# Kernel optimization log

Hardware: AMD Instinct MI355X
Metric: run time of the kernel (lower is better)

The kernel has to match this reference:

```python
import jax, jax.numpy as jnp
import numpy as np

N = 50000
E = 800000
IN, HID, OUT = 256, 64, 64
H1, H2 = 4, 1
SLOPE = 0.2  # DGL GATConv default negative_slope


def setup_inputs() -> dict:
    key = jax.random.key(0)
    ks = jax.random.split(key, 12)
    inp = {
        "features": jax.random.normal(ks[0], (N, IN), jnp.float32),
        "src": jax.random.randint(ks[1], (E,), 0, N),
        "dst": jax.random.randint(ks[2], (E,), 0, N),
        # layer 1 params (fc has no bias in DGL; separate bias added post-aggregation)
        "W1": jax.random.normal(ks[3], (IN, H1 * HID), jnp.float32) * (1.0 / np.sqrt(IN)),
        "al1": jax.random.normal(ks[4], (H1, HID), jnp.float32) * 0.1,
        "ar1": jax.random.normal(ks[5], (H1, HID), jnp.float32) * 0.1,
        "b1": jnp.zeros((H1 * HID,), jnp.float32),
        # layer 2 params
        "W2": jax.random.normal(ks[6], (H1 * HID, H2 * OUT), jnp.float32) * (1.0 / np.sqrt(H1 * HID)),
        "al2": jax.random.normal(ks[7], (H2, OUT), jnp.float32) * 0.1,
        "ar2": jax.random.normal(ks[8], (H2, OUT), jnp.float32) * 0.1,
        "b2": jnp.zeros((H2 * OUT,), jnp.float32),
    }
    return inp


def _gat_layer(x, src, dst, W, al, ar, b, H, D):
    # fc projection + reshape to [N, H, D]
    h = (x @ W).reshape(-1, H, D)
    el = jnp.einsum("nhd,hd->nh", h, al)  # [N,H]
    er = jnp.einsum("nhd,hd->nh", h, ar)
    e = jax.nn.leaky_relu(el[src] + er[dst], SLOPE)  # [E,H]
    # segment (per-dst-node) softmax over incoming edges
    emax = jax.ops.segment_max(e, dst, num_segments=N)
    ex = jnp.exp(e - emax[dst])
    denom = jax.ops.segment_sum(ex, dst, num_segments=N)
    a = ex / denom[dst]  # [E,H]
    # weighted gather-scatter aggregation
    out = jax.ops.segment_sum(a[:, :, None] * h[src], dst, num_segments=N)  # [N,H,D]
    return out + b.reshape(1, H, D)


def reference(features, src, dst, W1, al1, ar1, b1, W2, al2, ar2, b2):
    # layer 1: GATConv + elu activation, then flatten heads
    h = _gat_layer(features, src, dst, W1, al1, ar1, b1, H1, HID)
    h = jax.nn.elu(h).reshape(N, H1 * HID)
    # layer 2: GATConv (no activation), then mean over heads
    h = _gat_layer(h, src, dst, W2, al2, ar2, b2, H2, OUT)
    return h.mean(axis=1)  # [N, OUT]
```

## Files before the change

kernel.cpp:

```cpp
#include <hip/hip_runtime.h>
#include <hip/hip_bf16.h>
#include <hip/hip_fp16.h>
#include <math.h>

#define SLOPE 0.2f

typedef __attribute__((ext_vector_type(8))) short bf16x8;
typedef __attribute__((ext_vector_type(4))) float f32x4;

__device__ inline unsigned short f2bf(float f) {
    unsigned u = __float_as_uint(f);
    u += 0x7FFF + ((u >> 16) & 1);
    return (unsigned short)(u >> 16);
}
__device__ inline float bf2f(unsigned short s) {
    return __uint_as_float(((unsigned)s) << 16);
}
__device__ inline unsigned cvt_pk_bf16(float a, float b) {
    unsigned r;
    asm("v_cvt_pk_bf16_f32 %0, %1, %2" : "=v"(r) : "v"(a), "v"(b));
    return r;
}


__global__ void deg_kernel(const int* __restrict__ dst, int* __restrict__ deg,
                           int* __restrict__ rank, int E) {
    int i = blockIdx.x * blockDim.x + threadIdx.x;
    if (i < E) rank[i] = atomicAdd(&deg[dst[i]], 1);
}

__global__ __launch_bounds__(256) void psum_kernel(const int* __restrict__ deg,
                                                   int* __restrict__ bsum, int n) {
    const int t = threadIdx.x;
    const int i = blockIdx.x * 256 + t;
    int v = (i < n) ? deg[i] : 0;
#pragma unroll
    for (int o = 1; o < 64; o <<= 1) v += __shfl_xor(v, o, 64);
    __shared__ int ws[4];
    if ((t & 63) == 0) ws[t >> 6] = v;
    __syncthreads();
    if (t == 0) bsum[blockIdx.x] = ws[0] + ws[1] + ws[2] + ws[3];
}

__global__ __launch_bounds__(256) void scan2_kernel(const int* __restrict__ deg,
                                                    const int* __restrict__ bsum,
                                                    int* __restrict__ offs, int n) {
    const int b = blockIdx.x, t = threadIdx.x;
    const int lane = t & 63, w = t >> 6;

    int contrib = (t < b) ? bsum[t] : 0;
#pragma unroll
    for (int o = 1; o < 64; o <<= 1) contrib += __shfl_xor(contrib, o, 64);
    __shared__ int wsum[4];
    if (lane == 0) wsum[w] = contrib;
    __syncthreads();
    const int base = wsum[0] + wsum[1] + wsum[2] + wsum[3];

    const int i = b * 256 + t;
    const int v = (i < n) ? deg[i] : 0;
    int incl = v;
#pragma unroll
    for (int o = 1; o < 64; o <<= 1) {
        const int u = __shfl_up(incl, o, 64);
        if (lane >= o) incl += u;
    }
    __shared__ int wtot[4];
    if (lane == 63) wtot[w] = incl;
    __syncthreads();
    int wbase = 0;
#pragma unroll
    for (int k = 0; k < 4; ++k)
        if (k < w) wbase += wtot[k];

    const int excl = base + wbase + incl - v;
    if (i < n) offs[i] = excl;
    if (i == n - 1) offs[n] = excl + v;
}

__global__ void fill_kernel(const int* __restrict__ src, const int* __restrict__ dst,
                            const int* __restrict__ offs, const int* __restrict__ rank,
                            int* __restrict__ csr_src, int E) {
    int i = blockIdx.x * blockDim.x + threadIdx.x;
    if (i < E) {
        csr_src[offs[dst[i]] + rank[i]] = src[i];
    }
}

__global__ void cvt_w_kernel(const float* __restrict__ W1, const float* __restrict__ W2,
                             unsigned short* __restrict__ Wt1,
                             unsigned short* __restrict__ Wt2) {
    const int k = blockIdx.x, c = threadIdx.x;
    Wt1[c * 256 + k] = f2bf(W1[k * 256 + c]);
    if (c < 64) Wt2[c * 256 + k] = f2bf(W2[k * 64 + c]);
}

__global__ __launch_bounds__(256) void gemm1_mfma(const float* __restrict__ Xf,
                                                  const unsigned short* __restrict__ Wt,
                                                  const float* __restrict__ AL,
                                                  const float* __restrict__ AR,
                                                  unsigned short* __restrict__ Hout,
                                                  float* __restrict__ el,
                                                  float* __restrict__ er, int n) {
    constexpr int LDR = 72;
    __shared__ __align__(16) unsigned short Xs[128 * LDR];
    __shared__ __align__(16) unsigned short Ws[128 * LDR];

    const int tid = threadIdx.x;
    const int wave = tid >> 6, lane = tid & 63;
    const int col16 = lane & 15, quad = lane >> 4;
    const int node0 = blockIdx.x * 128;
    const int fb = blockIdx.y;

    f32x4 acc[8][2];
#pragma unroll
    for (int ft = 0; ft < 8; ++ft)
#pragma unroll
        for (int nt = 0; nt < 2; ++nt) acc[ft][nt] = (f32x4){0.f, 0.f, 0.f, 0.f};

    const int rr = tid >> 3;
    const int cc = (tid & 7) * 8;

    for (int k0 = 0; k0 < 256; k0 += 64) {
#pragma unroll
        for (int p = 0; p < 4; ++p) {
            const int row = rr + p * 32;
            int gx = node0 + row; if (gx >= n) gx = n - 1;
            const float4* xp = (const float4*)&Xf[(long long)gx * 256 + k0 + cc];
            const float4 a = xp[0];
            const float4 b = xp[1];
            uint4 pk;
            pk.x = cvt_pk_bf16(a.x, a.y);
            pk.y = cvt_pk_bf16(a.z, a.w);
            pk.z = cvt_pk_bf16(b.x, b.y);
            pk.w = cvt_pk_bf16(b.z, b.w);
            *(uint4*)&Xs[row * LDR + cc] = pk;
            *(bf16x8*)&Ws[row * LDR + cc] =
                *(const bf16x8*)&Wt[((long long)(fb * 128 + row)) * 256 + k0 + cc];
        }
        __syncthreads();
#pragma unroll
        for (int ks = 0; ks < 64; ks += 32) {
            bf16x8 bfrag[2];
#pragma unroll
            for (int nt = 0; nt < 2; ++nt)
                bfrag[nt] = *(const bf16x8*)&Xs[(wave * 32 + nt * 16 + col16) * LDR +
                                                ks + quad * 8];
#pragma unroll
            for (int ft = 0; ft < 8; ++ft) {
                const bf16x8 afrag =
                    *(const bf16x8*)&Ws[(ft * 16 + col16) * LDR + ks + quad * 8];
                acc[ft][0] = __builtin_amdgcn_mfma_f32_16x16x32_bf16(afrag, bfrag[0],
                                                                     acc[ft][0], 0, 0, 0);
                acc[ft][1] = __builtin_amdgcn_mfma_f32_16x16x32_bf16(afrag, bfrag[1],
                                                                     acc[ft][1], 0, 0, 0);
            }
        }
        __syncthreads();
    }

    float elp[2][2] = {{0.f, 0.f}, {0.f, 0.f}};
    float erp[2][2] = {{0.f, 0.f}, {0.f, 0.f}};
#pragma unroll
    for (int ft = 0; ft < 8; ++ft) {
        const int hb = ft >> 2;
        const int head = fb * 2 + hb;
        float alw[4], arw[4];
#pragma unroll
        for (int r = 0; r < 4; ++r) {
            const int d = (ft & 3) * 16 + quad * 4 + r;
            alw[r] = AL[head * 64 + d];
            arw[r] = AR[head * 64 + d];
        }
#pragma unroll
        for (int nt = 0; nt < 2; ++nt) {
            const int node = node0 + wave * 32 + nt * 16 + col16;
            if (node < n) {
                uint2 pk;
                pk.x = cvt_pk_bf16(acc[ft][nt][0], acc[ft][nt][1]);
                pk.y = cvt_pk_bf16(acc[ft][nt][2], acc[ft][nt][3]);
                *(uint2*)&Hout[(long long)node * 256 + fb * 128 + ft * 16 + quad * 4] = pk;
            }
#pragma unroll
            for (int r = 0; r < 4; ++r) {
                elp[nt][hb] = fmaf(acc[ft][nt][r], alw[r], elp[nt][hb]);
                erp[nt][hb] = fmaf(acc[ft][nt][r], arw[r], erp[nt][hb]);
            }
        }
    }
#pragma unroll
    for (int nt = 0; nt < 2; ++nt)
#pragma unroll
        for (int hb = 0; hb < 2; ++hb) {
            elp[nt][hb] += __shfl_xor(elp[nt][hb], 16, 64);
            elp[nt][hb] += __shfl_xor(elp[nt][hb], 32, 64);
            erp[nt][hb] += __shfl_xor(erp[nt][hb], 16, 64);
            erp[nt][hb] += __shfl_xor(erp[nt][hb], 32, 64);
        }
    if (quad == 0) {
#pragma unroll
        for (int nt = 0; nt < 2; ++nt) {
            const int node = node0 + wave * 32 + nt * 16 + col16;
            if (node < n) {
#pragma unroll
                for (int hb = 0; hb < 2; ++hb) {
                    el[node * 4 + fb * 2 + hb] = elp[nt][hb];
                    er[node * 4 + fb * 2 + hb] = erp[nt][hb];
                }
            }
        }
    }
}

__global__ __launch_bounds__(256) void gemm2_mfma(const unsigned short* __restrict__ Xbf,
                                                  const unsigned short* __restrict__ Wt,
                                                  const float* __restrict__ AL,
                                                  const float* __restrict__ AR,
                                                  unsigned short* __restrict__ Hout,
                                                  float* __restrict__ el,
                                                  float* __restrict__ er, int n) {
    constexpr int LDR = 72;
    __shared__ __align__(16) unsigned short Xs[128 * LDR];
    __shared__ __align__(16) unsigned short Ws[64 * LDR];

    const int tid = threadIdx.x;
    const int wave = tid >> 6, lane = tid & 63;
    const int col16 = lane & 15, quad = lane >> 4;
    const int node0 = blockIdx.x * 128;

    f32x4 acc[4][2];
#pragma unroll
    for (int ft = 0; ft < 4; ++ft)
#pragma unroll
        for (int nt = 0; nt < 2; ++nt) acc[ft][nt] = (f32x4){0.f, 0.f, 0.f, 0.f};

    const int rr = tid >> 3;
    const int cc = (tid & 7) * 8;

    for (int k0 = 0; k0 < 256; k0 += 64) {
#pragma unroll
        for (int p = 0; p < 4; ++p) {
            const int row = rr + p * 32;
            int gx = node0 + row; if (gx >= n) gx = n - 1;
            *(bf16x8*)&Xs[row * LDR + cc] =
                *(const bf16x8*)&Xbf[(long long)gx * 256 + k0 + cc];
        }
#pragma unroll
        for (int p = 0; p < 2; ++p) {
            const int row = rr + p * 32;
            *(bf16x8*)&Ws[row * LDR + cc] =
                *(const bf16x8*)&Wt[(long long)row * 256 + k0 + cc];
        }
        __syncthreads();
#pragma unroll
        for (int ks = 0; ks < 64; ks += 32) {
            bf16x8 bfrag[2];
#pragma unroll
            for (int nt = 0; nt < 2; ++nt)
                bfrag[nt] = *(const bf16x8*)&Xs[(wave * 32 + nt * 16 + col16) * LDR +
                                                ks + quad * 8];
#pragma unroll
            for (int ft = 0; ft < 4; ++ft) {
                const bf16x8 afrag =
                    *(const bf16x8*)&Ws[(ft * 16 + col16) * LDR + ks + quad * 8];
                acc[ft][0] = __builtin_amdgcn_mfma_f32_16x16x32_bf16(afrag, bfrag[0],
                                                                     acc[ft][0], 0, 0, 0);
                acc[ft][1] = __builtin_amdgcn_mfma_f32_16x16x32_bf16(afrag, bfrag[1],
                                                                     acc[ft][1], 0, 0, 0);
            }
        }
        __syncthreads();
    }

    float elp[2] = {0.f, 0.f}, erp[2] = {0.f, 0.f};
#pragma unroll
    for (int ft = 0; ft < 4; ++ft) {
        float alw[4], arw[4];
#pragma unroll
        for (int r = 0; r < 4; ++r) {
            const int d = ft * 16 + quad * 4 + r;
            alw[r] = AL[d];
            arw[r] = AR[d];
        }
#pragma unroll
        for (int nt = 0; nt < 2; ++nt) {
            const int node = node0 + wave * 32 + nt * 16 + col16;
            if (node < n) {
                ushort4 pk;
                pk.x = __half_as_ushort(__float2half(acc[ft][nt][0]));
                pk.y = __half_as_ushort(__float2half(acc[ft][nt][1]));
                pk.z = __half_as_ushort(__float2half(acc[ft][nt][2]));
                pk.w = __half_as_ushort(__float2half(acc[ft][nt][3]));
                *(ushort4*)&Hout[(long long)node * 64 + ft * 16 + quad * 4] = pk;
            }
#pragma unroll
            for (int r = 0; r < 4; ++r) {
                elp[nt] = fmaf(acc[ft][nt][r], alw[r], elp[nt]);
                erp[nt] = fmaf(acc[ft][nt][r], arw[r], erp[nt]);
            }
        }
    }
#pragma unroll
    for (int nt = 0; nt < 2; ++nt) {
        elp[nt] += __shfl_xor(elp[nt], 16, 64);
        elp[nt] += __shfl_xor(elp[nt], 32, 64);
        erp[nt] += __shfl_xor(erp[nt], 16, 64);
        erp[nt] += __shfl_xor(erp[nt], 32, 64);
    }
    if (quad == 0) {
#pragma unroll
        for (int nt = 0; nt < 2; ++nt) {
            const int node = node0 + wave * 32 + nt * 16 + col16;
            if (node < n) {
                el[node] = elp[nt];
                er[node] = erp[nt];
            }
        }
    }
}

__global__ __launch_bounds__(256) void aggr1_kernel(const unsigned short* __restrict__ Hf,
                                                    const float* __restrict__ el,
                                                    const float* __restrict__ er,
                                                    const int* __restrict__ offs,
                                                    const int* __restrict__ csr,
                                                    const float* __restrict__ bias,
                                                    unsigned short* __restrict__ out,
                                                    int n) {
    const int node = (blockIdx.x * blockDim.x + threadIdx.x) >> 6;
    if (node >= n) return;
    const int lane = threadIdx.x & 63;
    const int g = lane >> 4;
    const int r = lane & 15;
    const int h = r >> 2;
    const int beg = offs[node], end = offs[node + 1];
    const float erv = er[node * 4 + h];

    float acc[16];
#pragma unroll
    for (int q = 0; q < 16; ++q) acc[q] = 0.f;
    float l = 0.f;

    const int nb = (end - beg + 3) >> 2;
    int ci = beg + g; if (ci >= end) ci = end - 1;
    int s = csr[ci];
#pragma unroll 2
    for (int it = 0; it < nb; ++it) {
        const int ei = beg + it * 4 + g;
        const bool ok = ei < end;
        int nci = ei + 4; if (nci >= end) nci = end - 1;
        const int sn = csr[nci];
        float e = el[s * 4 + h] + erv;
        e = (e > 0.f) ? e : SLOPE * e;
        float p = __expf(fminf(e, 80.f));
        if (!ok) p = 0.f;
        const uint4* hp = (const uint4*)(Hf + (s << 8) + (r << 4));
        const uint4 u0 = hp[0];
        const uint4 u1 = hp[1];
        l += p;
        const unsigned uu[8] = {u0.x, u0.y, u0.z, u0.w, u1.x, u1.y, u1.z, u1.w};
#pragma unroll
        for (int q = 0; q < 8; ++q) {
            const float flo = __uint_as_float(uu[q] << 16);
            const float fhi = __uint_as_float(uu[q] & 0xFFFF0000u);
            acc[2 * q]     = fmaf(p, flo, acc[2 * q]);
            acc[2 * q + 1] = fmaf(p, fhi, acc[2 * q + 1]);
        }
        s = sn;
    }

#pragma unroll
    for (int q = 0; q < 16; ++q) {
        acc[q] += __shfl_xor(acc[q], 16, 64);
        acc[q] += __shfl_xor(acc[q], 32, 64);
    }
    l += __shfl_xor(l, 16, 64);
    l += __shfl_xor(l, 32, 64);

    if (g == 0) {
        const float inv = (l > 0.f) ? 1.f / l : 0.f;
        unsigned o[8];
#pragma unroll
        for (int q = 0; q < 8; ++q) {
            float v0 = acc[2 * q]     * inv + bias[r * 16 + 2 * q];
            float v1 = acc[2 * q + 1] * inv + bias[r * 16 + 2 * q + 1];
            v0 = (v0 > 0.f) ? v0 : expm1f(v0);
            v1 = (v1 > 0.f) ? v1 : expm1f(v1);
            o[q] = cvt_pk_bf16(v0, v1);
        }
        uint4* op = (uint4*)(out + (node << 8) + (r << 4));
        op[0] = make_uint4(o[0], o[1], o[2], o[3]);
        op[1] = make_uint4(o[4], o[5], o[6], o[7]);
    }
}

__global__ __launch_bounds__(256) void aggr2_kernel(const unsigned short* __restrict__ Hf,
                                                    const float* __restrict__ el,
                                                    const float* __restrict__ er,
                                                    const int* __restrict__ offs,
                                                    const int* __restrict__ csr,
                                                    const float* __restrict__ bias,
                                                    float* __restrict__ out, int n) {
    const int node = (blockIdx.x * blockDim.x + threadIdx.x) >> 6;
    if (node >= n) return;
    const int lane = threadIdx.x & 63;
    const int g = lane >> 4;
    const int r = lane & 15;
    const int beg = offs[node], end = offs[node + 1];
    const float erv = er[node];

    float a0 = 0.f, a1 = 0.f, a2 = 0.f, a3 = 0.f, l = 0.f;
    const int nb = (end - beg + 3) >> 2;
    int ci = beg + g; if (ci >= end) ci = end - 1;
    int s = csr[ci];
#pragma unroll 2
    for (int it = 0; it < nb; ++it) {
        const int ei = beg + it * 4 + g;
        const bool ok = ei < end;
        int nci = ei + 4; if (nci >= end) nci = end - 1;
        const int sn = csr[nci];
        float e = el[s] + erv;
        e = (e > 0.f) ? e : SLOPE * e;
        float p = __expf(fminf(e, 80.f));
        if (!ok) p = 0.f;
        const uint2 u = *(const uint2*)(Hf + (s << 6) + (r << 2));
        const float h0 = __half2float(__ushort_as_half((unsigned short)(u.x & 0xFFFFu)));
        const float h1 = __half2float(__ushort_as_half((unsigned short)(u.x >> 16)));
        const float h2 = __half2float(__ushort_as_half((unsigned short)(u.y & 0xFFFFu)));
        const float h3 = __half2float(__ushort_as_half((unsigned short)(u.y >> 16)));
        l += p;
        a0 = fmaf(p, h0, a0);
        a1 = fmaf(p, h1, a1);
        a2 = fmaf(p, h2, a2);
        a3 = fmaf(p, h3, a3);
        s = sn;
    }

    a0 += __shfl_xor(a0, 16, 64); a0 += __shfl_xor(a0, 32, 64);
    a1 += __shfl_xor(a1, 16, 64); a1 += __shfl_xor(a1, 32, 64);
    a2 += __shfl_xor(a2, 16, 64); a2 += __shfl_xor(a2, 32, 64);
    a3 += __shfl_xor(a3, 16, 64); a3 += __shfl_xor(a3, 32, 64);
    l  += __shfl_xor(l, 16, 64);  l  += __shfl_xor(l, 32, 64);

    if (g == 0) {
        const float inv = (l > 0.f) ? 1.f / l : 0.f;
        const float4 b4 = *(const float4*)(bias + r * 4);
        *(float4*)(out + (node << 6) + (r << 2)) =
            make_float4(fmaf(a0, inv, b4.x), fmaf(a1, inv, b4.y),
                        fmaf(a2, inv, b4.z), fmaf(a3, inv, b4.w));
    }
}


extern "C" void kernel_launch(void* const* d_in, const int* in_sizes, int n_in,
                              void* d_out, int out_size, void* d_ws, size_t ws_size,
                              hipStream_t stream) {
    const float* feat = (const float*)d_in[0];
    const int*   src  = (const int*)d_in[1];
    const int*   dst  = (const int*)d_in[2];
    const float* W1   = (const float*)d_in[3];
    const float* al1  = (const float*)d_in[4];
    const float* ar1  = (const float*)d_in[5];
    const float* b1   = (const float*)d_in[6];
    const float* W2   = (const float*)d_in[7];
    const float* al2  = (const float*)d_in[8];
    const float* ar2  = (const float*)d_in[9];
    const float* b2   = (const float*)d_in[10];
    float* out = (float*)d_out;

    const int IN = 256, HID = 64, OUT = 64, H1 = 4, H2 = 1;
    const int N = in_sizes[0] / IN;
    const int E = in_sizes[1];

    size_t off = 0;
    auto alloc = [&](size_t bytes) {
        void* p = (char*)d_ws + off;
        off += (bytes + 255) & ~(size_t)255;
        return p;
    };
    int*   deg    = (int*)alloc((size_t)N * 4);
    int*   offs   = (int*)alloc((size_t)(N + 1) * 4);
    int*   bsum   = (int*)alloc((size_t)256 * 4);
    int*   rank   = (int*)alloc((size_t)E * 4);
    int*   csr    = (int*)alloc((size_t)E * 4);
    unsigned short* h1   = (unsigned short*)alloc((size_t)N * H1 * HID * 2);
    unsigned short* wt1  = (unsigned short*)alloc((size_t)IN * H1 * HID * 2);
    unsigned short* wt2  = (unsigned short*)alloc((size_t)H1 * HID * H2 * OUT * 2);
    unsigned short* x2bf = (unsigned short*)alloc((size_t)N * H1 * HID * 2);
    unsigned short* h2   = (unsigned short*)alloc((size_t)N * H2 * OUT * 2);
    float* el1    = (float*)alloc((size_t)N * H1 * 4);
    float* er1    = (float*)alloc((size_t)N * H1 * 4);
    float* el2    = (float*)alloc((size_t)N * H2 * 4);
    float* er2    = (float*)alloc((size_t)N * H2 * 4);
    (void)ws_size;

    hipMemsetAsync(deg, 0, (size_t)N * 4, stream);

    const int nb = (N + 255) / 256;
    deg_kernel<<<(E + 255) / 256, 256, 0, stream>>>(dst, deg, rank, E);
    psum_kernel<<<nb, 256, 0, stream>>>(deg, bsum, N);
    scan2_kernel<<<nb, 256, 0, stream>>>(deg, bsum, offs, N);
    fill_kernel<<<(E + 255) / 256, 256, 0, stream>>>(src, dst, offs, rank, csr, E);

    cvt_w_kernel<<<256, 256, 0, stream>>>(W1, W2, wt1, wt2);

    {
        dim3 g((N + 127) / 128, 2);
        gemm1_mfma<<<g, 256, 0, stream>>>(feat, wt1, al1, ar1, h1, el1, er1, N);
    }
    aggr1_kernel<<<(N + 3) / 4, 256, 0, stream>>>(h1, el1, er1, offs, csr, b1, x2bf, N);
    gemm2_mfma<<<(N + 127) / 128, 256, 0, stream>>>(x2bf, wt2, al2, ar2, h2, el2, er2, N);
    aggr2_kernel<<<(N + 3) / 4, 256, 0, stream>>>(h2, el2, er2, offs, csr, b2, out, N);
}
```

Before: 299.3 us.

## Compute all four heads per gemm1 block and widen aggr2 loads

gemm1 drops its 2-way split over feature blocks, so each block now computes all 256 output columns. The fp32 feature tile is read and converted to bf16 once instead of twice, at the cost of doubling the accumulator registers (16x2 f32x4) and the weight LDS tile, which can lower occupancy. aggr2 now has each lane load 8 halves (uint4) instead of 4 and processes 8 edges per iteration with 8 lanes per row. This widens memory transactions and gives more edge-level parallelism per node, with one extra shuffle reduction step.

```diff
diff --git a/kernel.cpp b/kernel.cpp
--- a/kernel.cpp
+++ b/kernel.cpp
@@ -103,17 +103,16 @@
                                                   float* __restrict__ er, int n) {
     constexpr int LDR = 72;
     __shared__ __align__(16) unsigned short Xs[128 * LDR];
-    __shared__ __align__(16) unsigned short Ws[128 * LDR];
+    __shared__ __align__(16) unsigned short Ws[256 * LDR];
 
     const int tid = threadIdx.x;
     const int wave = tid >> 6, lane = tid & 63;
     const int col16 = lane & 15, quad = lane >> 4;
     const int node0 = blockIdx.x * 128;
-    const int fb = blockIdx.y;
-
-    f32x4 acc[8][2];
-#pragma unroll
-    for (int ft = 0; ft < 8; ++ft)
+
+    f32x4 acc[16][2];
+#pragma unroll
+    for (int ft = 0; ft < 16; ++ft)
 #pragma unroll
         for (int nt = 0; nt < 2; ++nt) acc[ft][nt] = (f32x4){0.f, 0.f, 0.f, 0.f};
 
@@ -134,8 +133,12 @@
             pk.z = cvt_pk_bf16(b.x, b.y);
             pk.w = cvt_pk_bf16(b.z, b.w);
             *(uint4*)&Xs[row * LDR + cc] = pk;
+        }
+#pragma unroll
+        for (int p = 0; p < 8; ++p) {
+            const int row = rr + p * 32;
             *(bf16x8*)&Ws[row * LDR + cc] =
-                *(const bf16x8*)&Wt[((long long)(fb * 128 + row)) * 256 + k0 + cc];
+                *(const bf16x8*)&Wt[(long long)row * 256 + k0 + cc];
         }
         __syncthreads();
 #pragma unroll
@@ -146,7 +149,7 @@
                 bfrag[nt] = *(const bf16x8*)&Xs[(wave * 32 + nt * 16 + col16) * LDR +
                                                 ks + quad * 8];
 #pragma unroll
-            for (int ft = 0; ft < 8; ++ft) {
+            for (int ft = 0; ft < 16; ++ft) {
                 const bf16x8 afrag =
                     *(const bf16x8*)&Ws[(ft * 16 + col16) * LDR + ks + quad * 8];
                 acc[ft][0] = __builtin_amdgcn_mfma_f32_16x16x32_bf16(afrag, bfrag[0],
@@ -158,18 +161,17 @@
         __syncthreads();
     }
 
-    float elp[2][2] = {{0.f, 0.f}, {0.f, 0.f}};
-    float erp[2][2] = {{0.f, 0.f}, {0.f, 0.f}};
-#pragma unroll
-    for (int ft = 0; ft < 8; ++ft) {
+    float elp[2][4] = {{0.f}, {0.f}};
+    float erp[2][4] = {{0.f}, {0.f}};
+#pragma unroll
+    for (int ft = 0; ft < 16; ++ft) {
         const int hb = ft >> 2;
-        const int head = fb * 2 + hb;
         float alw[4], arw[4];
 #pragma unroll
         for (int r = 0; r < 4; ++r) {
             const int d = (ft & 3) * 16 + quad * 4 + r;
-            alw[r] = AL[head * 64 + d];
-            arw[r] = AR[head * 64 + d];
+            alw[r] = AL[hb * 64 + d];
+            arw[r] = AR[hb * 64 + d];
         }
 #pragma unroll
         for (int nt = 0; nt < 2; ++nt) {
@@ -178,7 +180,7 @@
                 uint2 pk;
                 pk.x = cvt_pk_bf16(acc[ft][nt][0], acc[ft][nt][1]);
                 pk.y = cvt_pk_bf16(acc[ft][nt][2], acc[ft][nt][3]);
-                *(uint2*)&Hout[(long long)node * 256 + fb * 128 + ft * 16 + quad * 4] = pk;
+                *(uint2*)&Hout[(long long)node * 256 + ft * 16 + quad * 4] = pk;
             }
 #pragma unroll
             for (int r = 0; r < 4; ++r) {
@@ -190,7 +192,7 @@
 #pragma unroll
     for (int nt = 0; nt < 2; ++nt)
 #pragma unroll
-        for (int hb = 0; hb < 2; ++hb) {
+        for (int hb = 0; hb < 4; ++hb) {
             elp[nt][hb] += __shfl_xor(elp[nt][hb], 16, 64);
             elp[nt][hb] += __shfl_xor(elp[nt][hb], 32, 64);
             erp[nt][hb] += __shfl_xor(erp[nt][hb], 16, 64);
@@ -202,9 +204,9 @@
             const int node = node0 + wave * 32 + nt * 16 + col16;
             if (node < n) {
 #pragma unroll
-                for (int hb = 0; hb < 2; ++hb) {
-                    el[node * 4 + fb * 2 + hb] = elp[nt][hb];
-                    er[node * 4 + fb * 2 + hb] = erp[nt][hb];
+                for (int hb = 0; hb < 4; ++hb) {
+                    el[node * 4 + hb] = elp[nt][hb];
+                    er[node * 4 + hb] = erp[nt][hb];
                 }
             }
         }
@@ -403,50 +405,61 @@
     const int node = (blockIdx.x * blockDim.x + threadIdx.x) >> 6;
     if (node >= n) return;
     const int lane = threadIdx.x & 63;
-    const int g = lane >> 4;
-    const int r = lane & 15;
+    const int g = lane >> 3;
+    const int r = lane & 7;
     const int beg = offs[node], end = offs[node + 1];
     const float erv = er[node];
 
-    float a0 = 0.f, a1 = 0.f, a2 = 0.f, a3 = 0.f, l = 0.f;
-    const int nb = (end - beg + 3) >> 2;
+    float acc[8];
+#pragma unroll
+    for (int q = 0; q < 8; ++q) acc[q] = 0.f;
+    float l = 0.f;
+
+    const int nb = (end - beg + 7) >> 3;
     int ci = beg + g; if (ci >= end) ci = end - 1;
     int s = csr[ci];
 #pragma unroll 2
     for (int it = 0; it < nb; ++it) {
-        const int ei = beg + it * 4 + g;
+        const int ei = beg + it * 8 + g;
         const bool ok = ei < end;
-        int nci = ei + 4; if (nci >= end) nci = end - 1;
+        int nci = ei + 8; if (nci >= end) nci = end - 1;
         const int sn = csr[nci];
         float e = el[s] + erv;
         e = (e > 0.f) ? e : SLOPE * e;
         float p = __expf(fminf(e, 80.f));
         if (!ok) p = 0.f;
-        const uint2 u = *(const uint2*)(Hf + (s << 6) + (r << 2));
-        const float h0 = __half2float(__ushort_as_half((unsigned short)(u.x & 0xFFFFu)));
-        const float h1 = __half2float(__ushort_as_half((unsigned short)(u.x >> 16)));
-        const float h2 = __half2float(__ushort_as_half((unsigned short)(u.y & 0xFFFFu)));
-        const float h3 = __half2float(__ushort_as_half((unsigned short)(u.y >> 16)));
+        const uint4 u = *(const uint4*)(Hf + (s << 6) + (r << 3));
         l += p;
-        a0 = fmaf(p, h0, a0);
-        a1 = fmaf(p, h1, a1);
-        a2 = fmaf(p, h2, a2);
-        a3 = fmaf(p, h3, a3);
+        const unsigned uu[4] = {u.x, u.y, u.z, u.w};
+#pragma unroll
+        for (int q = 0; q < 4; ++q) {
+            const float hlo = __half2float(__ushort_as_half((unsigned short)(uu[q] & 0xFFFFu)));
+            const float hhi = __half2float(__ushort_as_half((unsigned short)(uu[q] >> 16)));
+            acc[2 * q]     = fmaf(p, hlo, acc[2 * q]);
+            acc[2 * q + 1] = fmaf(p, hhi, acc[2 * q + 1]);
+        }
         s = sn;
     }
 
-    a0 += __shfl_xor(a0, 16, 64); a0 += __shfl_xor(a0, 32, 64);
-    a1 += __shfl_xor(a1, 16, 64); a1 += __shfl_xor(a1, 32, 64);
-    a2 += __shfl_xor(a2, 16, 64); a2 += __shfl_xor(a2, 32, 64);
-    a3 += __shfl_xor(a3, 16, 64); a3 += __shfl_xor(a3, 32, 64);
-    l  += __shfl_xor(l, 16, 64);  l  += __shfl_xor(l, 32, 64);
+#pragma unroll
+    for (int q = 0; q < 8; ++q) {
+        acc[q] += __shfl_xor(acc[q], 8, 64);
+        acc[q] += __shfl_xor(acc[q], 16, 64);
+        acc[q] += __shfl_xor(acc[q], 32, 64);
+    }
+    l += __shfl_xor(l, 8, 64);
+    l += __shfl_xor(l, 16, 64);
+    l += __shfl_xor(l, 32, 64);
 
     if (g == 0) {
         const float inv = (l > 0.f) ? 1.f / l : 0.f;
-        const float4 b4 = *(const float4*)(bias + r * 4);
-        *(float4*)(out + (node << 6) + (r << 2)) =
-            make_float4(fmaf(a0, inv, b4.x), fmaf(a1, inv, b4.y),
-                        fmaf(a2, inv, b4.z), fmaf(a3, inv, b4.w));
+        const float4 b0 = *(const float4*)(bias + r * 8);
+        const float4 b1 = *(const float4*)(bias + r * 8 + 4);
+        float* op = out + (node << 6) + (r << 3);
+        *(float4*)op = make_float4(fmaf(acc[0], inv, b0.x), fmaf(acc[1], inv, b0.y),
+                                   fmaf(acc[2], inv, b0.z), fmaf(acc[3], inv, b0.w));
+        *(float4*)(op + 4) = make_float4(fmaf(acc[4], inv, b1.x), fmaf(acc[5], inv, b1.y),
+                                         fmaf(acc[6], inv, b1.z), fmaf(acc[7], inv, b1.w));
     }
 }
 
@@ -503,10 +516,7 @@
 
     cvt_w_kernel<<<256, 256, 0, stream>>>(W1, W2, wt1, wt2);
 
-    {
-        dim3 g((N + 127) / 128, 2);
-        gemm1_mfma<<<g, 256, 0, stream>>>(feat, wt1, al1, ar1, h1, el1, er1, N);
-    }
+    gemm1_mfma<<<(N + 127) / 128, 256, 0, stream>>>(feat, wt1, al1, ar1, h1, el1, er1, N);
     aggr1_kernel<<<(N + 3) / 4, 256, 0, stream>>>(h1, el1, er1, offs, csr, b1, x2bf, N);
     gemm2_mfma<<<(N + 127) / 128, 256, 0, stream>>>(x2bf, wt2, al2, ar2, h2, el2, er2, N);
     aggr2_kernel<<<(N + 3) / 4, 256, 0, stream>>>(h2, el2, er2, offs, csr, b2, out, N);
```

Result: faster. 288.7 us (-3.5%).
